# Kernel optimization log

Hardware: AMD Instinct MI355X
Metric: run time of the kernel (lower is better)

## Reference

```python
import jax, jax.numpy as jnp
import numpy as np

B, L, F = 4, 8192, 1024
H, D = 16, 64
EPS = 1e-6

def _phi(x):
    # ELU+1 positive feature map, standard for linear attention
    return jax.nn.elu(x) + 1.0

def setup_inputs() -> dict:
    key = jax.random.key(0)
    ks = jax.random.split(key, 6)
    s_in = 1.0
    s_w = 1.0 / np.sqrt(F)
    s_o = 1.0 / np.sqrt(H * D)
    return {
        "inputs_q": jax.random.normal(ks[0], (B, L, F), jnp.float32),
        "inputs_kv": jax.random.normal(ks[1], (B, L, F), jnp.float32),
        "Wq": jax.random.normal(ks[2], (F, H, D), jnp.float32) * s_w,
        "Wk": jax.random.normal(ks[3], (F, H, D), jnp.float32) * s_w,
        "Wv": jax.random.normal(ks[4], (F, H, D), jnp.float32) * s_w,
        "Wo": jax.random.normal(ks[5], (H, D, F), jnp.float32) * s_o,
    }

def reference(inputs_q, inputs_kv, Wq, Wk, Wv, Wo):
    # QKV projections (split-head kernels, no bias)
    q = jnp.einsum('bqf,fhd->bqhd', inputs_q, Wq)   # [B,Lq,H,D]
    k = jnp.einsum('bkf,fhd->bkhd', inputs_kv, Wk)  # [B,Lk,H,D]
    v = jnp.einsum('bkf,fhd->bkhd', inputs_kv, Wv)  # [B,Lk,H,D]

    qp = _phi(q)
    kp = _phi(k)

    # Linear attention: O = phi(q) @ (phi(k)^T V) / (phi(q) . sum_k phi(k))
    kv = jnp.einsum('bkhd,bkhe->bhde', kp, v)       # [B,H,D,D] small state
    ksum = jnp.sum(kp, axis=1)                       # [B,H,D]
    z = 1.0 / (jnp.einsum('bqhd,bhd->bqh', qp, ksum) + EPS)
    out = jnp.einsum('bqhd,bhde,bqh->bqhe', qp, kv, z)  # [B,Lq,H,D]

    # Output projection
    return jnp.einsum('bqhe,hef->bqf', out, Wo)      # [B,Lq,F]
```

## Files before the change

kernel.cpp:

```cpp
#include <hip/hip_runtime.h>
#include <hip/hip_fp16.h>
#include <math.h>

typedef _Float16 half8  __attribute__((ext_vector_type(8)));
typedef _Float16 half4v __attribute__((ext_vector_type(4)));
typedef float    floatx4 __attribute__((ext_vector_type(4)));

#define NB   4
#define LL   8192
#define FF   1024
#define HH   16
#define DD   64
#define MTOT 32768
#define KK   1024
#define NN   1024
#define ZSCALE 65536.0f

__device__ __forceinline__ void gload_lds16(const void* g, void* l) {
  __builtin_amdgcn_global_load_lds(
      (const __attribute__((address_space(1))) void*)g,
      (__attribute__((address_space(3))) void*)l, 16, 0, 0);
}

__device__ __forceinline__ float phi_act(float x) {
  return x > 0.f ? x + 1.f : __expf(x);
}

__global__ void k_cvt(const float* __restrict__ src, _Float16* __restrict__ dst, int n4) {
  int stride = gridDim.x * blockDim.x;
  for (int i = blockIdx.x * blockDim.x + threadIdx.x; i < n4; i += stride) {
    float4 v = reinterpret_cast<const float4*>(src)[i];
    half4v h;
    h[0] = (_Float16)v.x; h[1] = (_Float16)v.y; h[2] = (_Float16)v.z; h[3] = (_Float16)v.w;
    reinterpret_cast<half4v*>(dst)[i] = h;
  }
}

__global__ void k_cvt_t(const float* __restrict__ W0, const float* __restrict__ W1,
                        const float* __restrict__ W2,
                        _Float16* __restrict__ T0, _Float16* __restrict__ T1,
                        _Float16* __restrict__ T2) {
  __shared__ float tile[32][33];
  int bid = blockIdx.x;
  int w = bid >> 10, rem = bid & 1023;
  int ti = rem >> 5, tj = rem & 31;
  const float* src = (w == 0) ? W0 : (w == 1) ? W1 : W2;
  _Float16*    dst = (w == 0) ? T0 : (w == 1) ? T1 : T2;
  int t = threadIdx.x;
  int r = t >> 3, c4 = (t & 7) << 2;
  float4 v = *reinterpret_cast<const float4*>(&src[(size_t)(ti * 32 + r) * FF + tj * 32 + c4]);
  tile[r][c4 + 0] = v.x; tile[r][c4 + 1] = v.y; tile[r][c4 + 2] = v.z; tile[r][c4 + 3] = v.w;
  __syncthreads();
  half4v h;
  h[0] = (_Float16)tile[c4 + 0][r];
  h[1] = (_Float16)tile[c4 + 1][r];
  h[2] = (_Float16)tile[c4 + 2][r];
  h[3] = (_Float16)tile[c4 + 3][r];
  *reinterpret_cast<half4v*>(&dst[(size_t)(tj * 32 + r) * FF + ti * 32 + c4]) = h;
}


template<int MATB, int HALF>
__device__ __forceinline__ void stage_half(const _Float16* __restrict__ G, int row0,
                                           int col0, _Float16* plane, int tid) {
  #pragma unroll
  for (int is = 0; is < 2; ++is) {
    int lin = is * 8192 + tid * 16;
    int swz = lin ^ (((lin >> 7) & 7) << 4);
    int rp = swz >> 7;
    int kb = swz & 127;
    int row;
    if constexpr (MATB) row = (rp >> 5) * 64 + HALF * 32 + (rp & 31);
    else                row = (rp >> 6) * 128 + HALF * 64 + (rp & 63);
    gload_lds16(G + (size_t)(row0 + row) * 1024 + col0 + (kb >> 1),
                (char*)plane + lin);
  }
}

__device__ __forceinline__ half8 frag_read(const _Float16* plane, int rp, int kk, int lh) {
  int byte = rp * 128 + kk * 64 + lh * 16;
  byte ^= ((byte >> 7) & 7) << 4;
  return *(const half8*)((const char*)plane + byte);
}

template<int MH, int NH>
__device__ __forceinline__ void qreads(const _Float16* sm, int buf,
                                       half8 (&bA)[8], half8 (&bB)[2][4],
                                       int wr, int wc, int lr, int lh) {
  if constexpr (NH == 0) {
    const _Float16* Ap = sm + buf * 32768 + MH * 8192;
    #pragma unroll
    for (int m = 0; m < 4; ++m)
      #pragma unroll
      for (int kk = 0; kk < 2; ++kk)
        bA[m * 2 + kk] = frag_read(Ap, wr * 64 + m * 16 + lr, kk, lh);
  }
  if constexpr (MH == 0) {
    const _Float16* Bp = sm + buf * 32768 + 16384 + NH * 8192;
    #pragma unroll
    for (int n = 0; n < 2; ++n)
      #pragma unroll
      for (int kk = 0; kk < 2; ++kk)
        bB[NH][n * 2 + kk] = frag_read(Bp, wc * 32 + n * 16 + lr, kk, lh);
  }
}

template<int MH, int NH, bool VM4>
__device__ __forceinline__ void qmfma(half8 (&bA)[8], half8 (&bB)[2][4],
                                      floatx4 (&acc)[8][4]) {
  if constexpr (VM4) {
    asm volatile("s_waitcnt vmcnt(4)" ::: "memory");
  }
  __builtin_amdgcn_s_barrier();
  __builtin_amdgcn_s_setprio(1);
  #pragma unroll
  for (int m = 0; m < 4; ++m)
    #pragma unroll
    for (int n = 0; n < 2; ++n)
      #pragma unroll
      for (int kk = 0; kk < 2; ++kk)
        acc[MH * 4 + m][NH * 2 + n] = __builtin_amdgcn_mfma_f32_16x16x32_f16(
            bA[m * 2 + kk], bB[NH][n * 2 + kk], acc[MH * 4 + m][NH * 2 + n], 0, 0, 0);
  __builtin_amdgcn_s_setprio(0);
  __builtin_amdgcn_s_barrier();
}

template<int TBUF>
__device__ __forceinline__ void do_tile(int t, const _Float16* __restrict__ Ab,
                                        const _Float16* __restrict__ Bb,
                                        int i0, int j0, _Float16* sm, int tid,
                                        half8 (&bA)[8], half8 (&bB)[2][4],
                                        floatx4 (&acc)[8][4],
                                        int wr, int wc, int lr, int lh) {
  _Float16* self  = sm + TBUF * 32768;
  _Float16* other = sm + (TBUF ^ 1) * 32768;
  const int c1 = ((t + 1 < 16) ? (t + 1) : 15) * 64;
  const int c2 = ((t + 2 < 16) ? (t + 2) : 15) * 64;
  qreads<0, 0>(sm, TBUF, bA, bB, wr, wc, lr, lh);
  stage_half<1, 1>(Bb, j0, c1, other + 24576, tid);
  qmfma<0, 0, false>(bA, bB, acc);
  qreads<0, 1>(sm, TBUF, bA, bB, wr, wc, lr, lh);
  stage_half<0, 1>(Ab, i0, c1, other + 8192, tid);
  qmfma<0, 1, false>(bA, bB, acc);
  qreads<1, 0>(sm, TBUF, bA, bB, wr, wc, lr, lh);
  stage_half<0, 0>(Ab, i0, c2, self + 0, tid);
  qmfma<1, 0, false>(bA, bB, acc);
  stage_half<1, 0>(Bb, j0, c2, self + 16384, tid);
  qmfma<1, 1, true>(bA, bB, acc);
}

template<int MODE, bool PHI>
__global__ __launch_bounds__(512, 2)
void k_gemm(const _Float16* __restrict__ A, const _Float16* __restrict__ BT,
            void* __restrict__ Cptr, float* __restrict__ aux, float outScale) {
  __shared__ __align__(16) _Float16 smem[65536];
  const int tid  = threadIdx.x;
  const int lane = tid & 63;
  const int wid  = tid >> 6;
  const int wr = wid >> 2, wc = wid & 3;
  const int lr = lane & 15, lh = lane >> 4;

  constexpr int NT = (MODE == 1) ? 8 : 4;
  constexpr int CH = (MODE == 1) ? 128 : 64;
  const int tile = (blockIdx.x & 7) * CH + (blockIdx.x >> 3);
  const int tm = tile / NT, tn = tile % NT;
  const int i0 = tm * 256, j0 = tn * 256;

  const _Float16* Ab = A;
  const _Float16* Bb = (MODE == 2) ? BT + ((size_t)(i0 >> 13)) * ((size_t)NN * KK) : BT;

  floatx4 acc[8][4];
  #pragma unroll
  for (int m = 0; m < 8; ++m)
    #pragma unroll
    for (int n = 0; n < 4; ++n)
      #pragma unroll
      for (int r = 0; r < 4; ++r) acc[m][n][r] = 0.f;

  _Float16* sm = (_Float16*)smem;
  half8 bA[8];
  half8 bB[2][4];

  stage_half<0, 0>(Ab, i0, 0,  sm + 0,             tid);
  stage_half<1, 0>(Bb, j0, 0,  sm + 16384,         tid);
  stage_half<1, 1>(Bb, j0, 0,  sm + 24576,         tid);
  stage_half<0, 1>(Ab, i0, 0,  sm + 8192,          tid);
  stage_half<0, 0>(Ab, i0, 64, sm + 32768 + 0,     tid);
  stage_half<1, 0>(Bb, j0, 64, sm + 32768 + 16384, tid);
  asm volatile("s_waitcnt vmcnt(4)" ::: "memory");
  __builtin_amdgcn_s_barrier();

  #pragma unroll 1
  for (int tt = 0; tt < 8; ++tt) {
    do_tile<0>(2 * tt,     Ab, Bb, i0, j0, sm, tid, bA, bB, acc, wr, wc, lr, lh);
    do_tile<1>(2 * tt + 1, Ab, Bb, i0, j0, sm, tid, bA, bB, acc, wr, wc, lr, lh);
  }

  asm volatile("s_waitcnt vmcnt(0)" ::: "memory");
  __builtin_amdgcn_s_barrier();

  if constexpr (MODE == 0) {
    _Float16* C = (_Float16*)Cptr;
    #pragma unroll
    for (int m = 0; m < 8; ++m) {
      int row = i0 + wr * 128 + m * 16 + lh * 4;
      #pragma unroll
      for (int n = 0; n < 4; ++n) {
        int col = j0 + wc * 64 + n * 16 + lr;
        #pragma unroll
        for (int r = 0; r < 4; ++r) {
          float v = acc[m][n][r];
          if constexpr (PHI) v = phi_act(v);
          C[(size_t)(row + r) * NN + col] = (_Float16)v;
        }
      }
    }
  } else if constexpr (MODE == 2) {
    float* C = (float*)Cptr;
    #pragma unroll
    for (int m = 0; m < 8; ++m) {
      int row = i0 + wr * 128 + m * 16 + lh * 4;
      #pragma unroll
      for (int n = 0; n < 4; ++n) {
        int col = j0 + wc * 64 + n * 16 + lr;
        #pragma unroll
        for (int r = 0; r < 4; ++r)
          C[(size_t)(row + r) * NN + col] = acc[m][n][r] * outScale;
      }
    }
  } else {
    const int seg = j0 >> 10;
    const int j0s = j0 & 1023;
    const int bb  = i0 >> 13;
    const int l0  = i0 & 8191;
    float s[4] = {0.f, 0.f, 0.f, 0.f};
    #pragma unroll
    for (int m = 0; m < 8; ++m) {
      int l0l = wr * 128 + m * 16 + lh * 4;
      #pragma unroll
      for (int n = 0; n < 4; ++n) {
        int n_loc = wc * 64 + n * 16 + lr;
        int byte = (n_loc * 512 + l0l * 2) ^ ((n_loc & 7) << 4);
        half4v h;
        #pragma unroll
        for (int r = 0; r < 4; ++r) {
          float v = acc[m][n][r];
          if (seg == 0) { v = phi_act(v); s[n] += v; }
          h[r] = (_Float16)v;
        }
        *(half4v*)((char*)sm + byte) = h;
      }
    }
    if (seg == 0) {
      #pragma unroll
      for (int n = 0; n < 4; ++n) {
        s[n] += __shfl_xor(s[n], 16);
        s[n] += __shfl_xor(s[n], 32);
      }
      if (lh == 0) {
        int ch = (l0 >> 7) + wr;
        size_t base = ((size_t)bb * 64 + ch) * 1024 + j0s + wc * 64 + lr;
        #pragma unroll
        for (int n = 0; n < 4; ++n) aux[base + n * 16] = s[n];
      }
    }
    __syncthreads();
    _Float16* C = (_Float16*)Cptr;
    const size_t nbase = ((size_t)seg * 4 + bb) * 1024 + j0s;
    #pragma unroll 1
    for (int pass = 0; pass < 16; ++pass) {
      int n_loc = pass * 16 + (tid >> 5);
      int lo = (tid & 31) * 16;
      int byte = (n_loc * 512 + lo) ^ ((n_loc & 7) << 4);
      half8 v = *(const half8*)((char*)sm + byte);
      *(half8*)&C[(nbase + n_loc) * LL + l0 + (lo >> 1)] = v;
    }
  }
}

__global__ void k_ksum_red(const float* __restrict__ part, float* __restrict__ ksum) {
  int i = blockIdx.x * 256 + threadIdx.x;
  int b = i >> 10, col = i & 1023;
  float s = 0.f;
  for (int c = 0; c < 64; ++c) s += part[((size_t)b * 64 + c) * 1024 + col];
  ksum[i] = s;
}

__global__ __launch_bounds__(64)
void k_stageB(const _Float16* __restrict__ kpT, const _Float16* __restrict__ vT,
              float* __restrict__ kvpart) {
  __shared__ _Float16 Ak[64 * 72];
  __shared__ _Float16 Bv[64 * 72];
  const int bid = blockIdx.x;
  const int bh = bid >> 4, cc = bid & 15;
  const int lane = threadIdx.x;
  const int lr = lane & 15, lh = lane >> 4;
  const _Float16* Ab = kpT + (size_t)bh * 64 * LL + cc * 512;
  const _Float16* Bb = vT  + (size_t)bh * 64 * LL + cc * 512;

  floatx4 acc[4][4];
  #pragma unroll
  for (int m = 0; m < 4; ++m)
    #pragma unroll
    for (int n = 0; n < 4; ++n)
      #pragma unroll
      for (int r = 0; r < 4; ++r) acc[m][n][r] = 0.f;

  for (int kt = 0; kt < 512; kt += 64) {
    __syncthreads();
    #pragma unroll
    for (int j = 0; j < 8; ++j) {
      int chunk = lane + 64 * j;
      int rr = chunk >> 3;
      int off = (chunk & 7) * 8;
      *(half8*)&Ak[rr * 72 + off] = *(const half8*)&Ab[(size_t)rr * LL + kt + off];
      *(half8*)&Bv[rr * 72 + off] = *(const half8*)&Bb[(size_t)rr * LL + kt + off];
    }
    __syncthreads();
    #pragma unroll
    for (int ks = 0; ks < 2; ++ks) {
      half8 af[4], bf[4];
      #pragma unroll
      for (int m = 0; m < 4; ++m) af[m] = *(const half8*)&Ak[(m * 16 + lr) * 72 + ks * 32 + lh * 8];
      #pragma unroll
      for (int n = 0; n < 4; ++n) bf[n] = *(const half8*)&Bv[(n * 16 + lr) * 72 + ks * 32 + lh * 8];
      #pragma unroll
      for (int m = 0; m < 4; ++m)
        #pragma unroll
        for (int n = 0; n < 4; ++n)
          acc[m][n] = __builtin_amdgcn_mfma_f32_16x16x32_f16(af[m], bf[n], acc[m][n], 0, 0, 0);
    }
  }
  float* op = kvpart + (size_t)bid * 4096;
  #pragma unroll
  for (int m = 0; m < 4; ++m)
    #pragma unroll
    for (int n = 0; n < 4; ++n)
      #pragma unroll
      for (int r = 0; r < 4; ++r)
        op[(m * 16 + lh * 4 + r) * 64 + n * 16 + lr] = acc[m][n][r];
}

__global__ void k_reduce_kv(const float* __restrict__ kvpart, float* __restrict__ kv) {
  int gid = blockIdx.x * 256 + threadIdx.x;
  int bh = gid >> 12, i = gid & 4095;
  float s = 0.f;
  for (int c = 0; c < 16; ++c) s += kvpart[((size_t)bh * 16 + c) * 4096 + i];
  kv[gid] = s;
}

__global__ void k_zscale(_Float16* __restrict__ qp, const float* __restrict__ ksum) {
  int w = threadIdx.x >> 6, lane = threadIdx.x & 63;
  int row = blockIdx.x * 4 + w;
  int b = row >> 13;
  int h = lane >> 2;
  _Float16* p = qp + (size_t)row * 1024 + lane * 16;
  half8 v0 = *(half8*)&p[0];
  half8 v1 = *(half8*)&p[8];
  const float* ks = ksum + ((size_t)b * 16 + h) * 64 + (lane & 3) * 16;
  float dot = 0.f;
  #pragma unroll
  for (int e = 0; e < 8; ++e) dot += (float)v0[e] * ks[e];
  #pragma unroll
  for (int e = 0; e < 8; ++e) dot += (float)v1[e] * ks[8 + e];
  dot += __shfl_xor(dot, 1);
  dot += __shfl_xor(dot, 2);
  float zf = ZSCALE / (dot + 1e-6f);
  #pragma unroll
  for (int e = 0; e < 8; ++e) v0[e] = (_Float16)((float)v0[e] * zf);
  #pragma unroll
  for (int e = 0; e < 8; ++e) v1[e] = (_Float16)((float)v1[e] * zf);
  *(half8*)&p[0] = v0;
  *(half8*)&p[8] = v1;
}

__global__ __launch_bounds__(256)
void k_mker(const float* __restrict__ kv, const _Float16* __restrict__ Wo16,
            _Float16* __restrict__ MT) {
  __shared__ float kvs[4096];
  int bid = blockIdx.x;
  int fc = bid & 3, h = (bid >> 2) & 15, b = bid >> 6;
  const float* kvp = kv + ((size_t)b * 16 + h) * 4096;
  for (int i = threadIdx.x; i < 4096; i += 256) kvs[i] = kvp[i];
  __syncthreads();
  int f = fc * 256 + threadIdx.x;
  float acc[64];
  #pragma unroll
  for (int d = 0; d < 64; ++d) acc[d] = 0.f;
  for (int e = 0; e < 64; ++e) {
    float wv = (float)Wo16[(size_t)(h * 64 + e) * 1024 + f];
    #pragma unroll
    for (int d = 0; d < 64; ++d) acc[d] = fmaf(kvs[d * 64 + e], wv, acc[d]);
  }
  _Float16* op = MT + ((size_t)b * 1024 + f) * 1024 + h * 64;
  #pragma unroll
  for (int g = 0; g < 8; ++g) {
    half8 o;
    #pragma unroll
    for (int j = 0; j < 8; ++j) o[j] = (_Float16)acc[g * 8 + j];
    *(half8*)&op[g * 8] = o;
  }
}

extern "C" void kernel_launch(void* const* d_in, const int* in_sizes, int n_in,
                              void* d_out, int out_size, void* d_ws, size_t ws_size,
                              hipStream_t stream) {
  (void)in_sizes; (void)n_in; (void)out_size; (void)ws_size;
  const float* xq  = (const float*)d_in[0];
  const float* xkv = (const float*)d_in[1];
  const float* Wq  = (const float*)d_in[2];
  const float* Wk  = (const float*)d_in[3];
  const float* Wv  = (const float*)d_in[4];
  const float* Wo  = (const float*)d_in[5];

  char* ws = (char*)d_ws;
  _Float16* qp16 = (_Float16*)(ws + 0);
  _Float16* kpT  = (_Float16*)(ws + 67108864);
  _Float16* vT   = (_Float16*)(ws + 134217728);
  _Float16* WqT  = (_Float16*)(ws + 201326592);
  _Float16* WkT  = (_Float16*)(ws + 203423744);
  _Float16* WvT  = (_Float16*)(ws + 205520896);
  _Float16* Wo16 = (_Float16*)(ws + 207618048);
  float*    ksum = (float*)(ws + 209715200);
  float*    kv   = (float*)(ws + 209731584);
  float*    kvpart = (float*)(ws + 210780160);
  float*    ksum_part = (float*)(ws + 210780160);
  _Float16* MT   = (_Float16*)(ws + 227557376);

  _Float16* Xq16  = (_Float16*)d_out;
  _Float16* Xkv16 = Xq16 + 33554432;

  k_cvt<<<2048, 256, 0, stream>>>(xq,  Xq16,  8388608);
  k_cvt<<<2048, 256, 0, stream>>>(xkv, Xkv16, 8388608);
  k_cvt<<<512,  256, 0, stream>>>(Wo,  Wo16,  262144);
  k_cvt_t<<<3072, 256, 0, stream>>>(Wq, Wk, Wv, WqT, WkT, WvT);

  k_gemm<0, true ><<<512,  512, 0, stream>>>(Xq16,  WqT, qp16, nullptr,   1.0f);
  k_gemm<1, false><<<1024, 512, 0, stream>>>(Xkv16, WkT, kpT,  ksum_part, 1.0f);

  k_ksum_red<<<16, 256, 0, stream>>>(ksum_part, ksum);
  k_stageB<<<1024, 64, 0, stream>>>(kpT, vT, kvpart);
  k_reduce_kv<<<1024, 256, 0, stream>>>(kvpart, kv);

  k_zscale<<<8192, 256, 0, stream>>>(qp16, ksum);

  k_mker<<<256, 256, 0, stream>>>(kv, Wo16, MT);
  k_gemm<2, false><<<512, 512, 0, stream>>>(qp16, MT, d_out, nullptr, 1.0f / ZSCALE);
}
```

Before: 502.6 us.

## Fuse z-normalization into Q projection epilogue and merge input conversions

The Q projection GEMM now runs after the key-sum reduction and computes phi(q), its per-head dot with ksum via lane shuffles, and the scaled fp16 output directly in its epilogue. This removes the separate k_zscale pass, which re-read and re-wrote the full 64 MB qp buffer. The two input fp32-to-fp16 conversions are merged into one launch. The fused epilogue adds shuffles and a division per row, and it assumes each 16-lane shuffle group covers exactly one head's 64 columns.

Result: faster. 462.6 us (-7.9%).

```diff
diff --git a/kernel.cpp b/kernel.cpp
--- a/kernel.cpp
+++ b/kernel.cpp
@@ -24,6 +24,20 @@
 
 __device__ __forceinline__ float phi_act(float x) {
   return x > 0.f ? x + 1.f : __expf(x);
+}
+
+__global__ void k_cvt2(const float* __restrict__ a, const float* __restrict__ b,
+                       _Float16* __restrict__ da, _Float16* __restrict__ db, int n4each) {
+  int stride = gridDim.x * blockDim.x;
+  for (int i = blockIdx.x * blockDim.x + threadIdx.x; i < 2 * n4each; i += stride) {
+    const float* s; _Float16* d; int j;
+    if (i < n4each) { s = a; d = da; j = i; }
+    else            { s = b; d = db; j = i - n4each; }
+    float4 v = reinterpret_cast<const float4*>(s)[j];
+    half4v h;
+    h[0] = (_Float16)v.x; h[1] = (_Float16)v.y; h[2] = (_Float16)v.z; h[3] = (_Float16)v.w;
+    reinterpret_cast<half4v*>(d)[j] = h;
+  }
 }
 
 __global__ void k_cvt(const float* __restrict__ src, _Float16* __restrict__ dst, int n4) {
@@ -201,18 +215,31 @@
 
   if constexpr (MODE == 0) {
     _Float16* C = (_Float16*)Cptr;
+    const int bq = i0 >> 13;
+    float ks[4];
+    #pragma unroll
+    for (int n = 0; n < 4; ++n)
+      ks[n] = aux[(size_t)bq * 1024 + j0 + wc * 64 + n * 16 + lr];
     #pragma unroll
     for (int m = 0; m < 8; ++m) {
       int row = i0 + wr * 128 + m * 16 + lh * 4;
       #pragma unroll
-      for (int n = 0; n < 4; ++n) {
-        int col = j0 + wc * 64 + n * 16 + lr;
-        #pragma unroll
-        for (int r = 0; r < 4; ++r) {
-          float v = acc[m][n][r];
-          if constexpr (PHI) v = phi_act(v);
-          C[(size_t)(row + r) * NN + col] = (_Float16)v;
+      for (int r = 0; r < 4; ++r) {
+        float p[4];
+        float dot = 0.f;
+        #pragma unroll
+        for (int n = 0; n < 4; ++n) {
+          p[n] = phi_act(acc[m][n][r]);
+          dot = fmaf(p[n], ks[n], dot);
         }
+        dot += __shfl_xor(dot, 1);
+        dot += __shfl_xor(dot, 2);
+        dot += __shfl_xor(dot, 4);
+        dot += __shfl_xor(dot, 8);
+        float zf = ZSCALE / (dot + 1e-6f);
+        #pragma unroll
+        for (int n = 0; n < 4; ++n)
+          C[(size_t)(row + r) * NN + j0 + wc * 64 + n * 16 + lr] = (_Float16)(p[n] * zf);
       }
     }
   } else if constexpr (MODE == 2) {
@@ -347,31 +374,6 @@
   float s = 0.f;
   for (int c = 0; c < 16; ++c) s += kvpart[((size_t)bh * 16 + c) * 4096 + i];
   kv[gid] = s;
-}
-
-__global__ void k_zscale(_Float16* __restrict__ qp, const float* __restrict__ ksum) {
-  int w = threadIdx.x >> 6, lane = threadIdx.x & 63;
-  int row = blockIdx.x * 4 + w;
-  int b = row >> 13;
-  int h = lane >> 2;
-  _Float16* p = qp + (size_t)row * 1024 + lane * 16;
-  half8 v0 = *(half8*)&p[0];
-  half8 v1 = *(half8*)&p[8];
-  const float* ks = ksum + ((size_t)b * 16 + h) * 64 + (lane & 3) * 16;
-  float dot = 0.f;
-  #pragma unroll
-  for (int e = 0; e < 8; ++e) dot += (float)v0[e] * ks[e];
-  #pragma unroll
-  for (int e = 0; e < 8; ++e) dot += (float)v1[e] * ks[8 + e];
-  dot += __shfl_xor(dot, 1);
-  dot += __shfl_xor(dot, 2);
-  float zf = ZSCALE / (dot + 1e-6f);
-  #pragma unroll
-  for (int e = 0; e < 8; ++e) v0[e] = (_Float16)((float)v0[e] * zf);
-  #pragma unroll
-  for (int e = 0; e < 8; ++e) v1[e] = (_Float16)((float)v1[e] * zf);
-  *(half8*)&p[0] = v0;
-  *(half8*)&p[8] = v1;
 }
 
 __global__ __launch_bounds__(256)
@@ -430,20 +432,18 @@
   _Float16* Xq16  = (_Float16*)d_out;
   _Float16* Xkv16 = Xq16 + 33554432;
 
-  k_cvt<<<2048, 256, 0, stream>>>(xq,  Xq16,  8388608);
-  k_cvt<<<2048, 256, 0, stream>>>(xkv, Xkv16, 8388608);
-  k_cvt<<<512,  256, 0, stream>>>(Wo,  Wo16,  262144);
+  k_cvt2<<<4096, 256, 0, stream>>>(xq, xkv, Xq16, Xkv16, 8388608);
+  k_cvt<<<512,  256, 0, stream>>>(Wo, Wo16, 262144);
   k_cvt_t<<<3072, 256, 0, stream>>>(Wq, Wk, Wv, WqT, WkT, WvT);
 
-  k_gemm<0, true ><<<512,  512, 0, stream>>>(Xq16,  WqT, qp16, nullptr,   1.0f);
-  k_gemm<1, false><<<1024, 512, 0, stream>>>(Xkv16, WkT, kpT,  ksum_part, 1.0f);
-
+  k_gemm<1, false><<<1024, 512, 0, stream>>>(Xkv16, WkT, kpT, ksum_part, 1.0f);
   k_ksum_red<<<16, 256, 0, stream>>>(ksum_part, ksum);
+
   k_stageB<<<1024, 64, 0, stream>>>(kpT, vT, kvpart);
   k_reduce_kv<<<1024, 256, 0, stream>>>(kvpart, kv);
-
-  k_zscale<<<8192, 256, 0, stream>>>(qp16, ksum);
-
   k_mker<<<256, 256, 0, stream>>>(kv, Wo16, MT);
+
+  k_gemm<0, true><<<512, 512, 0, stream>>>(Xq16, WqT, qp16, ksum, 1.0f);
+
   k_gemm<2, false><<<512, 512, 0, stream>>>(qp16, MT, d_out, nullptr, 1.0f / ZSCALE);
 }
```
